# Kernel tuning notes

Hardware: AMD Instinct MI355X
Metric: run time of the kernel (lower is better)

Reference implementation:

```python
import jax, jax.numpy as jnp
import numpy as np

TOP_K = 8
NUM_EXPERTS = 256
NUM_GROUPS = 8
TOPK_GROUP = 4
SCALE = 2.5
EPS = 1e-20


def setup_inputs() -> dict:
    key = jax.random.key(0)
    k1, k2, k3 = jax.random.split(key, 3)
    T, H = 8192, 7168
    hidden_states = jax.random.normal(k1, (T, H), dtype=jnp.float32)
    # scale ~ kaiming-ish so logits are O(1) and sigmoid is not saturated
    weight = jax.random.normal(k2, (NUM_EXPERTS, H), dtype=jnp.float32) * (H ** -0.5)
    e_score_correction_bias = jax.random.normal(k3, (NUM_EXPERTS,), dtype=jnp.float32) * 0.1
    return {"hidden_states": hidden_states, "weight": weight,
            "e_score_correction_bias": e_score_correction_bias}


def reference(hidden_states, weight, e_score_correction_bias):
    T = hidden_states.shape[0]
    epg = NUM_EXPERTS // NUM_GROUPS  # experts per group
    # gating logits: [T, E]
    logits = jnp.einsum('th,eh->te', hidden_states.astype(jnp.float32),
                        weight.astype(jnp.float32))
    scores = jax.nn.sigmoid(logits)
    scores_for_choice = scores + e_score_correction_bias[None, :]
    # group score = sum of top-2 corrected scores within each group: [T, G]
    grouped = scores_for_choice.reshape(T, NUM_GROUPS, epg)
    top2, _ = jax.lax.top_k(grouped, 2)
    group_scores = top2.sum(axis=-1)
    # select topk_group groups, build mask [T, G]
    _, group_idx = jax.lax.top_k(group_scores, TOPK_GROUP)
    group_mask = jnp.zeros((T, NUM_GROUPS), dtype=scores.dtype)
    group_mask = group_mask.at[jnp.arange(T)[:, None], group_idx].set(1.0)
    # expand to expert mask [T, E]
    score_mask = jnp.repeat(group_mask, epg, axis=1)
    tmp_scores = jnp.where(score_mask > 0, scores_for_choice, 0.0)
    # top_k experts among allowed groups
    _, topk_idx = jax.lax.top_k(tmp_scores, TOP_K)
    # gather UNcorrected scores as weights
    topk_weight = jnp.take_along_axis(scores, topk_idx, axis=1)
    topk_weight = topk_weight / (topk_weight.sum(axis=-1, keepdims=True) + EPS)
    topk_weight = topk_weight * SCALE
    return topk_idx, topk_weight
```

## Files before the change

kernel.cpp:

```cpp
#include <hip/hip_runtime.h>
#include <cmath>

typedef __attribute__((ext_vector_type(8))) _Float16 half8;
typedef __attribute__((ext_vector_type(8))) unsigned short ushort8;
typedef __attribute__((ext_vector_type(4))) float f32x4;

#define HH 7168
#define NE 256
#define NQ 224
#define NITER 56
#define TOPK 8
#define TOPKG 4
#define WSC 1024.f
#define INV_WS (1.f/1024.f)
#define C1 (1.f/2048.f)
#define C2 (1.f/4194304.f)

__device__ __forceinline__ void split2(float x, unsigned short& h, unsigned short& m){
  const _Float16 hh = (_Float16)x;
  const float r = x - (float)hh;
  const _Float16 mm = (_Float16)(r * 2048.f);
  h = __builtin_bit_cast(unsigned short, hh);
  m = __builtin_bit_cast(unsigned short, mm);
}

__global__ __launch_bounds__(256) void prep_w(const float* __restrict__ wgt,
                                              unsigned short* __restrict__ bh,
                                              unsigned short* __restrict__ bm){
  const int b = blockIdx.x;
  const int nt = b & 15, qb = (b >> 4) * 4;
  const int w = threadIdx.x >> 6, L = threadIdx.x & 63;
  const int q = qb + w;
  const int e = nt*16 + (L & 15);
  const int k0 = 32*q + 8*(L >> 4);
  const float4 a0 = *(const float4*)(wgt + (size_t)e*HH + k0);
  const float4 a1 = *(const float4*)(wgt + (size_t)e*HH + k0 + 4);
  const float v[8] = {a0.x,a0.y,a0.z,a0.w,a1.x,a1.y,a1.z,a1.w};
  ushort8 h8, m8;
#pragma unroll
  for(int j=0;j<8;j++){ unsigned short hh,mm; split2(v[j]*WSC, hh, mm); h8[j]=hh; m8[j]=mm; }
  const size_t base = ((size_t)(q*16+nt)*64 + L)*8;
  *(ushort8*)(bh+base) = h8;
  *(ushort8*)(bm+base) = m8;
}

#define ABYTE(buf,lvl,mt,q,row) (((((buf)*2+(lvl))*8 + (mt)*4 + (q))*64 + (row))*16)
__device__ __forceinline__ int swz(int bo){ return bo ^ (((bo >> 8) & 7) << 4); }

__global__ __launch_bounds__(512,4)
void gemm(const float* __restrict__ hs,
          const unsigned short* __restrict__ bhp,
          const unsigned short* __restrict__ bmp,
          float* __restrict__ lgout){
  __shared__ __align__(16) unsigned short alds[16384];
  char* const aldsb = (char*)alds;

  const int tid = threadIdx.x, lane = tid & 63, w = tid >> 6;
  const int b = blockIdx.x;
  const int slice = (b >> 2) & 1;
  const int tg = (b >> 3)*4 + (b & 3);
  const int tb = tg*32, eb = slice*128;
  const int mtp = w >> 2, ntp = w & 3;

  const half8* __restrict__ bhv = (const half8*)bhp;
  const half8* __restrict__ bmv = (const half8*)bmp;

  f32x4 ksum[2], kcmp[2];
#pragma unroll
  for(int c=0;c<2;c++){ ksum[c]=f32x4{0,0,0,0}; kcmp[c]=f32x4{0,0,0,0}; }

  const int tokS = tid >> 4, kidx = tid & 15;
  const int mtS = tokS >> 4, m16S = tokS & 15;
  const int qS = kidx >> 2, kgS = kidx & 3;
  const int rowS = kgS*16 + m16S;
  const float* agp = hs + (size_t)(tb + tokS)*HH + kidx*8;

  float4 ga[2];
  ga[0] = *(const float4*)(agp);
  ga[1] = *(const float4*)(agp + 4);

  auto stage = [&](int buf){
    unsigned short h[8], m[8];
    const float* gv = (const float*)ga;
#pragma unroll
    for(int p=0;p<8;p++) split2(gv[p], h[p], m[p]);
    ushort8 h8, m8;
#pragma unroll
    for(int j=0;j<8;j++){ h8[j]=h[j]; m8[j]=m[j]; }
    *(ushort8*)(aldsb + swz(ABYTE(buf,0,mtS,qS,rowS))) = h8;
    *(ushort8*)(aldsb + swz(ABYTE(buf,1,mtS,qS,rowS))) = m8;
  };

  stage(0);
  half8 Bh[2], Bm[2];
#pragma unroll
  for(int ntl=0;ntl<2;ntl++){
    const int slot = ((0*16 + slice*8 + ntp*2 + ntl)*64 + lane);
    Bh[ntl] = bhv[slot]; Bm[ntl] = bmv[slot];
  }
  __syncthreads();

  for(int i=0;i<NITER;i++){
    const int cur = i & 1, nb = cur ^ 1;
    if(i+1 < NITER){
      const float* ap = agp + (size_t)(i+1)*128;
      ga[0] = *(const float4*)(ap);
      ga[1] = *(const float4*)(ap + 4);
    }
    f32x4 c0[2], c1[2], c2[2];
#pragma unroll
    for(int c=0;c<2;c++){ c0[c]=f32x4{0,0,0,0}; c1[c]=f32x4{0,0,0,0}; c2[c]=f32x4{0,0,0,0}; }

#pragma unroll
    for(int s=0;s<4;s++){
      const int q = i*4 + s;
      const half8 ah = *(const half8*)(aldsb + swz(ABYTE(cur,0,mtp,s,lane)));
      const half8 am = *(const half8*)(aldsb + swz(ABYTE(cur,1,mtp,s,lane)));
      half8 BhN[2], BmN[2];
      const bool more = (q+1 < NQ);
      if(more){
#pragma unroll
        for(int ntl=0;ntl<2;ntl++){
          const int slot = (((q+1)*16 + slice*8 + ntp*2 + ntl)*64 + lane);
          BhN[ntl] = bhv[slot]; BmN[ntl] = bmv[slot];
        }
      }
#pragma unroll
      for(int ntl=0;ntl<2;ntl++){
        c0[ntl] = __builtin_amdgcn_mfma_f32_16x16x32_f16(ah, Bh[ntl], c0[ntl], 0,0,0);
        c1[ntl] = __builtin_amdgcn_mfma_f32_16x16x32_f16(ah, Bm[ntl], c1[ntl], 0,0,0);
        c1[ntl] = __builtin_amdgcn_mfma_f32_16x16x32_f16(am, Bh[ntl], c1[ntl], 0,0,0);
        c2[ntl] = __builtin_amdgcn_mfma_f32_16x16x32_f16(am, Bm[ntl], c2[ntl], 0,0,0);
      }
      if(more){
#pragma unroll
        for(int ntl=0;ntl<2;ntl++){ Bh[ntl]=BhN[ntl]; Bm[ntl]=BmN[ntl]; }
      }
    }
    if(i+1 < NITER) stage(nb);
#pragma unroll
    for(int c=0;c<2;c++)
#pragma unroll
      for(int r=0;r<4;r++){
        const float v = c0[c][r] + c1[c][r]*C1 + c2[c][r]*C2;
        const float y = v - kcmp[c][r];
        const float t = ksum[c][r] + y;
        kcmp[c][r] = (t - ksum[c][r]) - y;
        ksum[c][r] = t;
      }
    __syncthreads();
  }

#pragma unroll
  for(int ntl=0;ntl<2;ntl++)
#pragma unroll
    for(int r=0;r<4;r++){
      const int tok = mtp*16 + (lane>>4)*4 + r;
      const int e = (ntp*2+ntl)*16 + (lane&15);
      const float lg = (ksum[ntl][r] - kcmp[ntl][r]) * INV_WS;
      lgout[(size_t)(tb+tok)*NE + eb + e] = lg;
    }
}

__global__ __launch_bounds__(256)
void gate(const float* __restrict__ lg, const float* __restrict__ bias,
          float* __restrict__ out, int T){
  const int tid = threadIdx.x, lane = tid & 63, wv = tid >> 6;
  const int t = blockIdx.x*4 + wv;
  const float4 bias4 = *(const float4*)(bias + 4*lane);
  const int g = lane >> 3;
  const float NEG_INF = -__builtin_inff();

  const float4 l4 = *(const float4*)(lg + (size_t)t*NE + 4*lane);
  float4 r4;
  r4.x = 1.f/(1.f + expf(-l4.x));
  r4.y = 1.f/(1.f + expf(-l4.y));
  r4.z = 1.f/(1.f + expf(-l4.z));
  r4.w = 1.f/(1.f + expf(-l4.w));
  float4 s4;
  s4.x = r4.x + bias4.x; s4.y = r4.y + bias4.y;
  s4.z = r4.z + bias4.z; s4.w = r4.w + bias4.w;

  float m1 = s4.x, m2 = NEG_INF;
  if (s4.y > m1) { m2 = m1; m1 = s4.y; } else if (s4.y > m2) m2 = s4.y;
  if (s4.z > m1) { m2 = m1; m1 = s4.z; } else if (s4.z > m2) m2 = s4.z;
  if (s4.w > m1) { m2 = m1; m1 = s4.w; } else if (s4.w > m2) m2 = s4.w;
#pragma unroll
  for (int m = 1; m <= 4; m <<= 1) {
    const float o1 = __shfl_xor(m1, m);
    const float o2 = __shfl_xor(m2, m);
    const float nm1 = fmaxf(m1, o1);
    const float nm2 = fmaxf(fminf(m1, o1), fmaxf(m2, o2));
    m1 = nm1; m2 = nm2;
  }
  const float gs = m1 + m2;

  float gsv[8];
#pragma unroll
  for (int j = 0; j < 8; ++j) gsv[j] = __shfl(gs, j * 8);

  unsigned gm = 0;
#pragma unroll
  for (int r = 0; r < TOPKG; ++r) {
    float best = NEG_INF; int bj = 0;
#pragma unroll
    for (int j = 0; j < 8; ++j) {
      const bool avail = !((gm >> j) & 1u);
      if (avail && gsv[j] > best) { best = gsv[j]; bj = j; }
    }
    gm |= 1u << bj;
  }
  const bool allowed = (gm >> g) & 1u;

  float v0 = allowed ? s4.x : 0.f;
  float v1 = allowed ? s4.y : 0.f;
  float v2 = allowed ? s4.z : 0.f;
  float v3 = allowed ? s4.w : 0.f;

  float sumw = 0.f;
  int myidx = 0; float myraw = 0.f;
#pragma unroll
  for (int r = 0; r < TOPK; ++r) {
    float bv = v0; int bj = 0;
    if (v1 > bv) { bv = v1; bj = 1; }
    if (v2 > bv) { bv = v2; bj = 2; }
    if (v3 > bv) { bv = v3; bj = 3; }
    int bidx = 4 * lane + bj;
#pragma unroll
    for (int m = 1; m < 64; m <<= 1) {
      const float ov = __shfl_xor(bv, m);
      const int   oi = __shfl_xor(bidx, m);
      if (ov > bv || (ov == bv && oi < bidx)) { bv = ov; bidx = oi; }
    }
    const int oj = bidx & 3;
    const float cand = (oj == 0) ? r4.x
                     : (oj == 1) ? r4.y
                     : (oj == 2) ? r4.z
                     :             r4.w;
    const float raw = __shfl(cand, bidx >> 2);
    sumw += raw;
    if (lane == r) { myidx = bidx; myraw = raw; }
    if (lane == (bidx >> 2)) {
      if      (oj == 0) v0 = NEG_INF;
      else if (oj == 1) v1 = NEG_INF;
      else if (oj == 2) v2 = NEG_INF;
      else              v3 = NEG_INF;
    }
  }

  if (lane < TOPK) {
    out[(size_t)t * TOPK + lane] = (float)myidx;
    out[(size_t)T * TOPK + (size_t)t * TOPK + lane] = myraw / (sumw + 1e-20f) * 2.5f;
  }
}

extern "C" void kernel_launch(void* const* d_in, const int* in_sizes, int n_in,
                              void* d_out, int out_size, void* d_ws, size_t ws_size,
                              hipStream_t stream) {
  const float* hs   = (const float*)d_in[0];
  const float* wgt  = (const float*)d_in[1];
  const float* bias = (const float*)d_in[2];
  float* out = (float*)d_out;

  const int T = in_sizes[0] / HH;

  unsigned short* bh = (unsigned short*)d_ws;
  unsigned short* bm = bh + (size_t)NE*HH;
  float* lgbuf = (float*)(bm + (size_t)NE*HH);

  hipLaunchKernelGGL(prep_w, dim3(896), dim3(256), 0, stream, wgt, bh, bm);
  hipLaunchKernelGGL(gemm,   dim3(512), dim3(512), 0, stream, hs, bh, bm, lgbuf);
  hipLaunchKernelGGL(gate,   dim3(T/4), dim3(256), 0, stream, lgbuf, bias, out, T);
}
```

Before: 465.2 us.

## Stage B operand through LDS via global_load_lds with finer K steps

The pre-split weight operand is now copied directly from global memory into a double-buffered 64KB LDS region with global_load_lds, and MFMA reads B from LDS instead of holding per-wave register prefetches. The K step per iteration is halved (NITER doubled), only half the threads convert and stage A, and MFMA sections are wrapped in s_setprio. The aim is to cut register pressure and redundant global B loads across waves, at the cost of much more LDS per block (80KB), which likely limits occupancy, and twice as many barriers.

After: 457.7 us. Within noise of the previous version (-1.6%).

```diff
diff --git a/kernel.cpp b/kernel.cpp
--- a/kernel.cpp
+++ b/kernel.cpp
@@ -8,7 +8,7 @@
 #define HH 7168
 #define NE 256
 #define NQ 224
-#define NITER 56
+#define NITER 112
 #define TOPK 8
 #define TOPKG 4
 #define WSC 1024.f
@@ -44,16 +44,23 @@
   *(ushort8*)(bm+base) = m8;
 }
 
-#define ABYTE(buf,lvl,mt,q,row) (((((buf)*2+(lvl))*8 + (mt)*4 + (q))*64 + (row))*16)
+#define ABYTE(buf,lvl,mt,q,row) ((((((buf)*2+(lvl))*2+(mt))*2+(q))*64+(row))*16)
+#define BBYTE(buf,lvl,q,nt) ((((buf)*4+(lvl)*2+(q))*8+(nt))<<10)
 __device__ __forceinline__ int swz(int bo){ return bo ^ (((bo >> 8) & 7) << 4); }
+
+__device__ __forceinline__ void glds16(const void* g, void* l){
+  __builtin_amdgcn_global_load_lds(
+      (const __attribute__((address_space(1))) unsigned int*)g,
+      (__attribute__((address_space(3))) unsigned int*)l, 16, 0, 0);
+}
 
 __global__ __launch_bounds__(512,4)
 void gemm(const float* __restrict__ hs,
           const unsigned short* __restrict__ bhp,
           const unsigned short* __restrict__ bmp,
           float* __restrict__ lgout){
-  __shared__ __align__(16) unsigned short alds[16384];
-  char* const aldsb = (char*)alds;
+  __shared__ __align__(16) unsigned char blds[65536];
+  __shared__ __align__(16) unsigned char alds[16384];
 
   const int tid = threadIdx.x, lane = tid & 63, w = tid >> 6;
   const int b = blockIdx.x;
@@ -62,69 +69,75 @@
   const int tb = tg*32, eb = slice*128;
   const int mtp = w >> 2, ntp = w & 3;
 
-  const half8* __restrict__ bhv = (const half8*)bhp;
-  const half8* __restrict__ bmv = (const half8*)bmp;
-
-  f32x4 ksum[2], kcmp[2];
+  f32x4 ksum[2], kcmp[2], c0[2], c1[2], c2[2];
 #pragma unroll
   for(int c=0;c<2;c++){ ksum[c]=f32x4{0,0,0,0}; kcmp[c]=f32x4{0,0,0,0}; }
 
-  const int tokS = tid >> 4, kidx = tid & 15;
+  const int tokS = (tid & 255) >> 3, kidx = tid & 7;
   const int mtS = tokS >> 4, m16S = tokS & 15;
   const int qS = kidx >> 2, kgS = kidx & 3;
   const int rowS = kgS*16 + m16S;
   const float* agp = hs + (size_t)(tb + tokS)*HH + kidx*8;
 
-  float4 ga[2];
-  ga[0] = *(const float4*)(agp);
-  ga[1] = *(const float4*)(agp + 4);
-
-  auto stage = [&](int buf){
+  auto stage = [&](int buf, const float4* g){
     unsigned short h[8], m[8];
-    const float* gv = (const float*)ga;
+    const float* gv = (const float*)g;
 #pragma unroll
     for(int p=0;p<8;p++) split2(gv[p], h[p], m[p]);
     ushort8 h8, m8;
 #pragma unroll
     for(int j=0;j<8;j++){ h8[j]=h[j]; m8[j]=m[j]; }
-    *(ushort8*)(aldsb + swz(ABYTE(buf,0,mtS,qS,rowS))) = h8;
-    *(ushort8*)(aldsb + swz(ABYTE(buf,1,mtS,qS,rowS))) = m8;
+    *(ushort8*)&alds[swz(ABYTE(buf,0,mtS,qS,rowS))] = h8;
+    *(ushort8*)&alds[swz(ABYTE(buf,1,mtS,qS,rowS))] = m8;
   };
 
-  stage(0);
-  half8 Bh[2], Bm[2];
-#pragma unroll
-  for(int ntl=0;ntl<2;ntl++){
-    const int slot = ((0*16 + slice*8 + ntp*2 + ntl)*64 + lane);
-    Bh[ntl] = bhv[slot]; Bm[ntl] = bmv[slot];
-  }
+  auto bstage = [&](int buf, int q32base){
+#pragma unroll
+    for(int j=0;j<4;j++){
+      const int sid = w*4 + j;
+      const int lvl = sid >> 4, q = (sid >> 3) & 1, nt = sid & 7;
+      const int q32 = q32base + q;
+      const unsigned short* src = (lvl ? bmp : bhp)
+          + ((size_t)((q32*16 + slice*8 + nt)*64 + lane))*8;
+      glds16(src, &blds[BBYTE(buf,lvl,q,nt)]);
+    }
+  };
+
+  float4 ga[2];
+  if(tid < 256){
+    ga[0] = *(const float4*)(agp);
+    ga[1] = *(const float4*)(agp + 4);
+  }
+  bstage(0, 0);
+  if(tid < 256) stage(0, ga);
   __syncthreads();
 
   for(int i=0;i<NITER;i++){
     const int cur = i & 1, nb = cur ^ 1;
-    if(i+1 < NITER){
-      const float* ap = agp + (size_t)(i+1)*128;
-      ga[0] = *(const float4*)(ap);
-      ga[1] = *(const float4*)(ap + 4);
-    }
-    f32x4 c0[2], c1[2], c2[2];
-#pragma unroll
-    for(int c=0;c<2;c++){ c0[c]=f32x4{0,0,0,0}; c1[c]=f32x4{0,0,0,0}; c2[c]=f32x4{0,0,0,0}; }
-
-#pragma unroll
-    for(int s=0;s<4;s++){
-      const int q = i*4 + s;
-      const half8 ah = *(const half8*)(aldsb + swz(ABYTE(cur,0,mtp,s,lane)));
-      const half8 am = *(const half8*)(aldsb + swz(ABYTE(cur,1,mtp,s,lane)));
-      half8 BhN[2], BmN[2];
-      const bool more = (q+1 < NQ);
-      if(more){
-#pragma unroll
-        for(int ntl=0;ntl<2;ntl++){
-          const int slot = (((q+1)*16 + slice*8 + ntp*2 + ntl)*64 + lane);
-          BhN[ntl] = bhv[slot]; BmN[ntl] = bmv[slot];
-        }
+    const bool more = (i+1 < NITER);
+    if(more){
+      if(tid < 256){
+        const float* ap = agp + (size_t)(i+1)*64;
+        ga[0] = *(const float4*)(ap);
+        ga[1] = *(const float4*)(ap + 4);
       }
+      bstage(nb, 2*(i+1));
+    }
+    if((i & 1) == 0){
+#pragma unroll
+      for(int c=0;c<2;c++){ c0[c]=f32x4{0,0,0,0}; c1[c]=f32x4{0,0,0,0}; c2[c]=f32x4{0,0,0,0}; }
+    }
+#pragma unroll
+    for(int s=0;s<2;s++){
+      const half8 ah = *(const half8*)&alds[swz(ABYTE(cur,0,mtp,s,lane))];
+      const half8 am = *(const half8*)&alds[swz(ABYTE(cur,1,mtp,s,lane))];
+      half8 Bh[2], Bm[2];
+#pragma unroll
+      for(int ntl=0;ntl<2;ntl++){
+        Bh[ntl] = *(const half8*)&blds[BBYTE(cur,0,s,ntp*2+ntl) + lane*16];
+        Bm[ntl] = *(const half8*)&blds[BBYTE(cur,1,s,ntp*2+ntl) + lane*16];
+      }
+      __builtin_amdgcn_s_setprio(1);
 #pragma unroll
       for(int ntl=0;ntl<2;ntl++){
         c0[ntl] = __builtin_amdgcn_mfma_f32_16x16x32_f16(ah, Bh[ntl], c0[ntl], 0,0,0);
@@ -132,22 +145,21 @@
         c1[ntl] = __builtin_amdgcn_mfma_f32_16x16x32_f16(am, Bh[ntl], c1[ntl], 0,0,0);
         c2[ntl] = __builtin_amdgcn_mfma_f32_16x16x32_f16(am, Bm[ntl], c2[ntl], 0,0,0);
       }
-      if(more){
-#pragma unroll
-        for(int ntl=0;ntl<2;ntl++){ Bh[ntl]=BhN[ntl]; Bm[ntl]=BmN[ntl]; }
-      }
-    }
-    if(i+1 < NITER) stage(nb);
-#pragma unroll
-    for(int c=0;c<2;c++)
-#pragma unroll
-      for(int r=0;r<4;r++){
-        const float v = c0[c][r] + c1[c][r]*C1 + c2[c][r]*C2;
-        const float y = v - kcmp[c][r];
-        const float t = ksum[c][r] + y;
-        kcmp[c][r] = (t - ksum[c][r]) - y;
-        ksum[c][r] = t;
-      }
+      __builtin_amdgcn_s_setprio(0);
+    }
+    if(more && tid < 256) stage(nb, ga);
+    if(i & 1){
+#pragma unroll
+      for(int c=0;c<2;c++)
+#pragma unroll
+        for(int r=0;r<4;r++){
+          const float v = c0[c][r] + c1[c][r]*C1 + c2[c][r]*C2;
+          const float y = v - kcmp[c][r];
+          const float t = ksum[c][r] + y;
+          kcmp[c][r] = (t - ksum[c][r]) - y;
+          ksum[c][r] = t;
+        }
+    }
     __syncthreads();
   }
 
```

## Stream B tiles into LDS via async global_load_lds with triple buffering

Applied to the files above, without the earlier changes.

The GEMM now loads the pre-split weight fragments (B) straight into shared memory with global_load_lds into a 3-stage ring buffer, instead of prefetching them into registers. Explicit vmcnt/lgkmcnt waits and raw barriers replace __syncthreads, and MFMA sections are wrapped in s_setprio. The aim is to hide global-load latency, cut register pressure and share B reads across waves through LDS. In exchange, LDS use grows to about 80KB per block, which may limit occupancy under launch_bounds(512,4), and the hand-written waitcnt sequencing could introduce races.

New measurement: 456.8 us. No clear change (-1.8%).

```diff
diff --git a/kernel.cpp b/kernel.cpp
--- a/kernel.cpp
+++ b/kernel.cpp
@@ -8,7 +8,7 @@
 #define HH 7168
 #define NE 256
 #define NQ 224
-#define NITER 56
+#define NWND 56
 #define TOPK 8
 #define TOPKG 4
 #define WSC 1024.f
@@ -44,16 +44,40 @@
   *(ushort8*)(bm+base) = m8;
 }
 
-#define ABYTE(buf,lvl,mt,q,row) (((((buf)*2+(lvl))*8 + (mt)*4 + (q))*64 + (row))*16)
+#define AB(aw,lvl,mt,q,row) (((((aw)*4+(lvl)*2+(mt))*4+(q))*64+(row))*16)
 __device__ __forceinline__ int swz(int bo){ return bo ^ (((bo >> 8) & 7) << 4); }
+
+__device__ __forceinline__ void glds16(const void* g, void* l){
+  __builtin_amdgcn_global_load_lds(
+      (const __attribute__((address_space(1))) unsigned int*)g,
+      (__attribute__((address_space(3))) unsigned int*)l, 16, 0, 0);
+}
+
+#define BAR_V4  do{ asm volatile("s_waitcnt vmcnt(4)" ::: "memory"); __builtin_amdgcn_s_barrier(); __builtin_amdgcn_sched_barrier(0); }while(0)
+#define BAR_V2  do{ asm volatile("s_waitcnt vmcnt(2)" ::: "memory"); __builtin_amdgcn_s_barrier(); __builtin_amdgcn_sched_barrier(0); }while(0)
+#define BAR_V2L do{ asm volatile("s_waitcnt lgkmcnt(0)\n\ts_waitcnt vmcnt(2)" ::: "memory"); __builtin_amdgcn_s_barrier(); __builtin_amdgcn_sched_barrier(0); }while(0)
+#define BAR_V0  do{ asm volatile("s_waitcnt vmcnt(0)" ::: "memory"); __builtin_amdgcn_s_barrier(); __builtin_amdgcn_sched_barrier(0); }while(0)
+
+#define KAHAN do{ \
+  _Pragma("unroll") \
+  for(int cc=0;cc<2;cc++) \
+    _Pragma("unroll") \
+    for(int r=0;r<4;r++){ \
+      const float v = c0[cc][r] + c1[cc][r]*C1 + c2[cc][r]*C2; \
+      const float y = v - kcmp[cc][r]; \
+      const float t = ksum[cc][r] + y; \
+      kcmp[cc][r] = (t - ksum[cc][r]) - y; \
+      ksum[cc][r] = t; \
+    } \
+}while(0)
 
 __global__ __launch_bounds__(512,4)
 void gemm(const float* __restrict__ hs,
           const unsigned short* __restrict__ bhp,
           const unsigned short* __restrict__ bmp,
           float* __restrict__ lgout){
-  __shared__ __align__(16) unsigned short alds[16384];
-  char* const aldsb = (char*)alds;
+  __shared__ __align__(16) unsigned char blds[49152];
+  __shared__ __align__(16) unsigned char alds[32768];
 
   const int tid = threadIdx.x, lane = tid & 63, w = tid >> 6;
   const int b = blockIdx.x;
@@ -62,24 +86,18 @@
   const int tb = tg*32, eb = slice*128;
   const int mtp = w >> 2, ntp = w & 3;
 
-  const half8* __restrict__ bhv = (const half8*)bhp;
-  const half8* __restrict__ bmv = (const half8*)bmp;
-
-  f32x4 ksum[2], kcmp[2];
-#pragma unroll
-  for(int c=0;c<2;c++){ ksum[c]=f32x4{0,0,0,0}; kcmp[c]=f32x4{0,0,0,0}; }
+  f32x4 ksum[2], kcmp[2], c0[2], c1[2], c2[2];
+#pragma unroll
+  for(int cc=0;cc<2;cc++){ ksum[cc]=f32x4{0,0,0,0}; kcmp[cc]=f32x4{0,0,0,0}; }
 
   const int tokS = tid >> 4, kidx = tid & 15;
   const int mtS = tokS >> 4, m16S = tokS & 15;
   const int qS = kidx >> 2, kgS = kidx & 3;
   const int rowS = kgS*16 + m16S;
   const float* agp = hs + (size_t)(tb + tokS)*HH + kidx*8;
-
   float4 ga[2];
-  ga[0] = *(const float4*)(agp);
-  ga[1] = *(const float4*)(agp + 4);
-
-  auto stage = [&](int buf){
+
+  auto stage = [&](int aw){
     unsigned short h[8], m[8];
     const float* gv = (const float*)ga;
 #pragma unroll
@@ -87,68 +105,99 @@
     ushort8 h8, m8;
 #pragma unroll
     for(int j=0;j<8;j++){ h8[j]=h[j]; m8[j]=m[j]; }
-    *(ushort8*)(aldsb + swz(ABYTE(buf,0,mtS,qS,rowS))) = h8;
-    *(ushort8*)(aldsb + swz(ABYTE(buf,1,mtS,qS,rowS))) = m8;
+    *(ushort8*)&alds[swz(AB(aw,0,mtS,qS,rowS))] = h8;
+    *(ushort8*)&alds[swz(AB(aw,1,mtS,qS,rowS))] = m8;
   };
 
+  const unsigned short* bsrc = (w >= 4 ? bmp : bhp)
+      + ((size_t)((slice*8 + (w&3)*2)*64 + lane))*8;
+  const int bdst = (w>>2)*8192 + (w&3)*2048;
+  auto issueB = [&](int bufoff, int qpre){
+    const unsigned short* s0 = bsrc + (size_t)qpre*8192;
+    glds16(s0,       &blds[bufoff + bdst]);
+    glds16(s0 + 512, &blds[bufoff + bdst + 1024]);
+  };
+
+  auto compute = [&](int awr, int q, int bc){
+    const half8 ah = *(const half8*)&alds[swz(AB(awr,0,mtp,q,lane))];
+    const half8 am = *(const half8*)&alds[swz(AB(awr,1,mtp,q,lane))];
+    half8 Bh[2], Bm[2];
+#pragma unroll
+    for(int ntl=0;ntl<2;ntl++){
+      Bh[ntl] = *(const half8*)&blds[bc + (ntp*2+ntl)*1024 + lane*16];
+      Bm[ntl] = *(const half8*)&blds[bc + 8192 + (ntp*2+ntl)*1024 + lane*16];
+    }
+    __builtin_amdgcn_s_setprio(1);
+#pragma unroll
+    for(int ntl=0;ntl<2;ntl++){
+      c0[ntl] = __builtin_amdgcn_mfma_f32_16x16x32_f16(ah, Bh[ntl], c0[ntl], 0,0,0);
+      c1[ntl] = __builtin_amdgcn_mfma_f32_16x16x32_f16(ah, Bm[ntl], c1[ntl], 0,0,0);
+      c1[ntl] = __builtin_amdgcn_mfma_f32_16x16x32_f16(am, Bh[ntl], c1[ntl], 0,0,0);
+      c2[ntl] = __builtin_amdgcn_mfma_f32_16x16x32_f16(am, Bm[ntl], c2[ntl], 0,0,0);
+    }
+    __builtin_amdgcn_s_setprio(0);
+  };
+
+  ga[0] = *(const float4*)agp; ga[1] = *(const float4*)(agp+4);
+  issueB(0,     0);
+  issueB(16384, 1);
   stage(0);
-  half8 Bh[2], Bm[2];
-#pragma unroll
-  for(int ntl=0;ntl<2;ntl++){
-    const int slot = ((0*16 + slice*8 + ntp*2 + ntl)*64 + lane);
-    Bh[ntl] = bhv[slot]; Bm[ntl] = bmv[slot];
-  }
-  __syncthreads();
-
-  for(int i=0;i<NITER;i++){
-    const int cur = i & 1, nb = cur ^ 1;
-    if(i+1 < NITER){
-      const float* ap = agp + (size_t)(i+1)*128;
-      ga[0] = *(const float4*)(ap);
-      ga[1] = *(const float4*)(ap + 4);
-    }
-    f32x4 c0[2], c1[2], c2[2];
-#pragma unroll
-    for(int c=0;c<2;c++){ c0[c]=f32x4{0,0,0,0}; c1[c]=f32x4{0,0,0,0}; c2[c]=f32x4{0,0,0,0}; }
-
-#pragma unroll
-    for(int s=0;s<4;s++){
-      const int q = i*4 + s;
-      const half8 ah = *(const half8*)(aldsb + swz(ABYTE(cur,0,mtp,s,lane)));
-      const half8 am = *(const half8*)(aldsb + swz(ABYTE(cur,1,mtp,s,lane)));
-      half8 BhN[2], BmN[2];
-      const bool more = (q+1 < NQ);
-      if(more){
-#pragma unroll
-        for(int ntl=0;ntl<2;ntl++){
-          const int slot = (((q+1)*16 + slice*8 + ntp*2 + ntl)*64 + lane);
-          BhN[ntl] = bhv[slot]; BmN[ntl] = bmv[slot];
-        }
-      }
-#pragma unroll
-      for(int ntl=0;ntl<2;ntl++){
-        c0[ntl] = __builtin_amdgcn_mfma_f32_16x16x32_f16(ah, Bh[ntl], c0[ntl], 0,0,0);
-        c1[ntl] = __builtin_amdgcn_mfma_f32_16x16x32_f16(ah, Bm[ntl], c1[ntl], 0,0,0);
-        c1[ntl] = __builtin_amdgcn_mfma_f32_16x16x32_f16(am, Bh[ntl], c1[ntl], 0,0,0);
-        c2[ntl] = __builtin_amdgcn_mfma_f32_16x16x32_f16(am, Bm[ntl], c2[ntl], 0,0,0);
-      }
-      if(more){
-#pragma unroll
-        for(int ntl=0;ntl<2;ntl++){ Bh[ntl]=BhN[ntl]; Bm[ntl]=BmN[ntl]; }
-      }
-    }
-    if(i+1 < NITER) stage(nb);
-#pragma unroll
-    for(int c=0;c<2;c++)
-#pragma unroll
-      for(int r=0;r<4;r++){
-        const float v = c0[c][r] + c1[c][r]*C1 + c2[c][r]*C2;
-        const float y = v - kcmp[c][r];
-        const float t = ksum[c][r] + y;
-        kcmp[c][r] = (t - ksum[c][r]) - y;
-        ksum[c][r] = t;
-      }
-    __syncthreads();
+  asm volatile("s_waitcnt lgkmcnt(0)\n\ts_waitcnt vmcnt(2)" ::: "memory");
+  __builtin_amdgcn_s_barrier();
+  __builtin_amdgcn_sched_barrier(0);
+
+  int bc = 0;
+#pragma unroll 1
+  for(int wnd=0; wnd<NWND-1; ++wnd){
+    const int i0 = wnd*4;
+    const int awr = wnd & 1, aws = awr ^ 1;
+    int bp;
+    bp = bc + 32768; if(bp >= 49152) bp -= 49152;
+    issueB(bp, i0+2);
+    { const float* ap = agp + (size_t)(wnd+1)*128;
+      ga[0] = *(const float4*)ap; ga[1] = *(const float4*)(ap+4); }
+#pragma unroll
+    for(int cc=0;cc<2;cc++){ c0[cc]=f32x4{0,0,0,0}; c1[cc]=f32x4{0,0,0,0}; c2[cc]=f32x4{0,0,0,0}; }
+    compute(awr, 0, bc);
+    BAR_V4;
+    bc += 16384; if(bc == 49152) bc = 0;
+    bp = bc + 32768; if(bp >= 49152) bp -= 49152;
+    issueB(bp, i0+3);
+    compute(awr, 1, bc);
+    BAR_V4;
+    bc += 16384; if(bc == 49152) bc = 0;
+    bp = bc + 32768; if(bp >= 49152) bp -= 49152;
+    issueB(bp, i0+4);
+    compute(awr, 2, bc);
+    stage(aws);
+    BAR_V2L;
+    bc += 16384; if(bc == 49152) bc = 0;
+    bp = bc + 32768; if(bp >= 49152) bp -= 49152;
+    issueB(bp, i0+5);
+    compute(awr, 3, bc);
+    KAHAN;
+    BAR_V2;
+    bc += 16384; if(bc == 49152) bc = 0;
+  }
+  {
+    int bp;
+    bp = bc + 32768; if(bp >= 49152) bp -= 49152;
+    issueB(bp, 222);
+#pragma unroll
+    for(int cc=0;cc<2;cc++){ c0[cc]=f32x4{0,0,0,0}; c1[cc]=f32x4{0,0,0,0}; c2[cc]=f32x4{0,0,0,0}; }
+    compute(1, 0, bc);
+    BAR_V2;
+    bc += 16384; if(bc == 49152) bc = 0;
+    bp = bc + 32768; if(bp >= 49152) bp -= 49152;
+    issueB(bp, 223);
+    compute(1, 1, bc);
+    BAR_V2;
+    bc += 16384; if(bc == 49152) bc = 0;
+    compute(1, 2, bc);
+    BAR_V0;
+    bc += 16384; if(bc == 49152) bc = 0;
+    compute(1, 3, bc);
+    KAHAN;
   }
 
 #pragma unroll
```

## Halve K-step per barrier, ping-pong B prefetch, and prioritize MFMA issue

Applied to the files above, without the earlier changes.

Each main-loop iteration now covers 64 K elements instead of 128, so the LDS A buffer holds two K-subtiles per stage instead of four. The loop count doubles and the Kahan accumulation runs every other iteration. B fragments are double-buffered in named registers (PA/PB) so the next subtile's global loads are issued before the current MFMAs run. MFMA groups are wrapped in s_setprio, and the full __syncthreads is replaced by an explicit lgkmcnt wait plus s_barrier, with the loop kept rolled. The aim is lower register and LDS pressure and better load/compute overlap, at the cost of twice as many barriers per K.

After: 486.2 us. +4.5%, slower.

```diff
diff --git a/kernel.cpp b/kernel.cpp
--- a/kernel.cpp
+++ b/kernel.cpp
@@ -8,7 +8,7 @@
 #define HH 7168
 #define NE 256
 #define NQ 224
-#define NITER 56
+#define NITER 112
 #define TOPK 8
 #define TOPKG 4
 #define WSC 1024.f
@@ -44,16 +44,41 @@
   *(ushort8*)(bm+base) = m8;
 }
 
-#define ABYTE(buf,lvl,mt,q,row) (((((buf)*2+(lvl))*8 + (mt)*4 + (q))*64 + (row))*16)
+#define AB(buf,lvl,mt,q,row) ((((((buf)*2+(lvl))*2+(mt))*2+(q))*64+(row))*16)
 __device__ __forceinline__ int swz(int bo){ return bo ^ (((bo >> 8) & 7) << 4); }
+
+#define KAHAN do{ \
+  _Pragma("unroll") \
+  for(int cc=0;cc<2;cc++) \
+    _Pragma("unroll") \
+    for(int r=0;r<4;r++){ \
+      const float v = c0[cc][r] + c1[cc][r]*C1 + c2[cc][r]*C2; \
+      const float y = v - kcmp[cc][r]; \
+      const float t = ksum[cc][r] + y; \
+      kcmp[cc][r] = (t - ksum[cc][r]) - y; \
+      ksum[cc][r] = t; \
+    } \
+}while(0)
+
+#define MFMA8(AH,AM,BH0,BH1,BM0,BM1) do{ \
+  __builtin_amdgcn_s_setprio(1); \
+  c0[0] = __builtin_amdgcn_mfma_f32_16x16x32_f16(AH, BH0, c0[0], 0,0,0); \
+  c1[0] = __builtin_amdgcn_mfma_f32_16x16x32_f16(AH, BM0, c1[0], 0,0,0); \
+  c1[0] = __builtin_amdgcn_mfma_f32_16x16x32_f16(AM, BH0, c1[0], 0,0,0); \
+  c2[0] = __builtin_amdgcn_mfma_f32_16x16x32_f16(AM, BM0, c2[0], 0,0,0); \
+  c0[1] = __builtin_amdgcn_mfma_f32_16x16x32_f16(AH, BH1, c0[1], 0,0,0); \
+  c1[1] = __builtin_amdgcn_mfma_f32_16x16x32_f16(AH, BM1, c1[1], 0,0,0); \
+  c1[1] = __builtin_amdgcn_mfma_f32_16x16x32_f16(AM, BH1, c1[1], 0,0,0); \
+  c2[1] = __builtin_amdgcn_mfma_f32_16x16x32_f16(AM, BM1, c2[1], 0,0,0); \
+  __builtin_amdgcn_s_setprio(0); \
+}while(0)
 
 __global__ __launch_bounds__(512,4)
 void gemm(const float* __restrict__ hs,
           const unsigned short* __restrict__ bhp,
           const unsigned short* __restrict__ bmp,
           float* __restrict__ lgout){
-  __shared__ __align__(16) unsigned short alds[16384];
-  char* const aldsb = (char*)alds;
+  __shared__ __align__(16) unsigned char alds[16384];
 
   const int tid = threadIdx.x, lane = tid & 63, w = tid >> 6;
   const int b = blockIdx.x;
@@ -62,22 +87,16 @@
   const int tb = tg*32, eb = slice*128;
   const int mtp = w >> 2, ntp = w & 3;
 
-  const half8* __restrict__ bhv = (const half8*)bhp;
-  const half8* __restrict__ bmv = (const half8*)bmp;
-
-  f32x4 ksum[2], kcmp[2];
-#pragma unroll
-  for(int c=0;c<2;c++){ ksum[c]=f32x4{0,0,0,0}; kcmp[c]=f32x4{0,0,0,0}; }
-
-  const int tokS = tid >> 4, kidx = tid & 15;
+  f32x4 ksum[2], kcmp[2], c0[2], c1[2], c2[2];
+#pragma unroll
+  for(int cc=0;cc<2;cc++){ ksum[cc]=f32x4{0,0,0,0}; kcmp[cc]=f32x4{0,0,0,0}; }
+
+  const int tokS = (tid & 255) >> 3, kidx = tid & 7;
   const int mtS = tokS >> 4, m16S = tokS & 15;
   const int qS = kidx >> 2, kgS = kidx & 3;
   const int rowS = kgS*16 + m16S;
   const float* agp = hs + (size_t)(tb + tokS)*HH + kidx*8;
-
   float4 ga[2];
-  ga[0] = *(const float4*)(agp);
-  ga[1] = *(const float4*)(agp + 4);
 
   auto stage = [&](int buf){
     unsigned short h[8], m[8];
@@ -87,68 +106,62 @@
     ushort8 h8, m8;
 #pragma unroll
     for(int j=0;j<8;j++){ h8[j]=h[j]; m8[j]=m[j]; }
-    *(ushort8*)(aldsb + swz(ABYTE(buf,0,mtS,qS,rowS))) = h8;
-    *(ushort8*)(aldsb + swz(ABYTE(buf,1,mtS,qS,rowS))) = m8;
+    *(ushort8*)&alds[swz(AB(buf,0,mtS,qS,rowS))] = h8;
+    *(ushort8*)&alds[swz(AB(buf,1,mtS,qS,rowS))] = m8;
   };
 
+  const half8* __restrict__ bhv = (const half8*)bhp;
+  const half8* __restrict__ bmv = (const half8*)bmp;
+  const int bbase0 = (slice*8 + ntp*2)*64 + lane;
+  const int bbase1 = bbase0 + 64;
+
+  ga[0] = *(const float4*)(agp);
+  ga[1] = *(const float4*)(agp + 4);
   stage(0);
-  half8 Bh[2], Bm[2];
-#pragma unroll
-  for(int ntl=0;ntl<2;ntl++){
-    const int slot = ((0*16 + slice*8 + ntp*2 + ntl)*64 + lane);
-    Bh[ntl] = bhv[slot]; Bm[ntl] = bmv[slot];
-  }
-  __syncthreads();
-
+  half8 PAh0 = bhv[bbase0], PAh1 = bhv[bbase1];
+  half8 PAm0 = bmv[bbase0], PAm1 = bmv[bbase1];
+  asm volatile("s_waitcnt lgkmcnt(0)" ::: "memory");
+  __builtin_amdgcn_s_barrier();
+
+  half8 PBh0, PBh1, PBm0, PBm1;
+
+#pragma unroll 1
   for(int i=0;i<NITER;i++){
     const int cur = i & 1, nb = cur ^ 1;
-    if(i+1 < NITER){
-      const float* ap = agp + (size_t)(i+1)*128;
+    const bool more = (i+1 < NITER);
+    if(more){
+      const float* ap = agp + (size_t)(i+1)*64;
       ga[0] = *(const float4*)(ap);
       ga[1] = *(const float4*)(ap + 4);
     }
-    f32x4 c0[2], c1[2], c2[2];
-#pragma unroll
-    for(int c=0;c<2;c++){ c0[c]=f32x4{0,0,0,0}; c1[c]=f32x4{0,0,0,0}; c2[c]=f32x4{0,0,0,0}; }
-
-#pragma unroll
-    for(int s=0;s<4;s++){
-      const int q = i*4 + s;
-      const half8 ah = *(const half8*)(aldsb + swz(ABYTE(cur,0,mtp,s,lane)));
-      const half8 am = *(const half8*)(aldsb + swz(ABYTE(cur,1,mtp,s,lane)));
-      half8 BhN[2], BmN[2];
-      const bool more = (q+1 < NQ);
-      if(more){
-#pragma unroll
-        for(int ntl=0;ntl<2;ntl++){
-          const int slot = (((q+1)*16 + slice*8 + ntp*2 + ntl)*64 + lane);
-          BhN[ntl] = bhv[slot]; BmN[ntl] = bmv[slot];
-        }
-      }
-#pragma unroll
-      for(int ntl=0;ntl<2;ntl++){
-        c0[ntl] = __builtin_amdgcn_mfma_f32_16x16x32_f16(ah, Bh[ntl], c0[ntl], 0,0,0);
-        c1[ntl] = __builtin_amdgcn_mfma_f32_16x16x32_f16(ah, Bm[ntl], c1[ntl], 0,0,0);
-        c1[ntl] = __builtin_amdgcn_mfma_f32_16x16x32_f16(am, Bh[ntl], c1[ntl], 0,0,0);
-        c2[ntl] = __builtin_amdgcn_mfma_f32_16x16x32_f16(am, Bm[ntl], c2[ntl], 0,0,0);
-      }
-      if(more){
-#pragma unroll
-        for(int ntl=0;ntl<2;ntl++){ Bh[ntl]=BhN[ntl]; Bm[ntl]=BmN[ntl]; }
-      }
-    }
-    if(i+1 < NITER) stage(nb);
-#pragma unroll
-    for(int c=0;c<2;c++)
-#pragma unroll
-      for(int r=0;r<4;r++){
-        const float v = c0[c][r] + c1[c][r]*C1 + c2[c][r]*C2;
-        const float y = v - kcmp[c][r];
-        const float t = ksum[c][r] + y;
-        kcmp[c][r] = (t - ksum[c][r]) - y;
-        ksum[c][r] = t;
-      }
-    __syncthreads();
+    if((i & 1) == 0){
+#pragma unroll
+      for(int cc=0;cc<2;cc++){ c0[cc]=f32x4{0,0,0,0}; c1[cc]=f32x4{0,0,0,0}; c2[cc]=f32x4{0,0,0,0}; }
+    }
+    {
+      const int s1 = (2*i+1)*1024;
+      PBh0 = bhv[s1 + bbase0]; PBh1 = bhv[s1 + bbase1];
+      PBm0 = bmv[s1 + bbase0]; PBm1 = bmv[s1 + bbase1];
+    }
+    {
+      const half8 ah = *(const half8*)&alds[swz(AB(cur,0,mtp,0,lane))];
+      const half8 am = *(const half8*)&alds[swz(AB(cur,1,mtp,0,lane))];
+      MFMA8(ah, am, PAh0, PAh1, PAm0, PAm1);
+    }
+    if(more){
+      const int s2 = (2*i+2)*1024;
+      PAh0 = bhv[s2 + bbase0]; PAh1 = bhv[s2 + bbase1];
+      PAm0 = bmv[s2 + bbase0]; PAm1 = bmv[s2 + bbase1];
+    }
+    {
+      const half8 ah = *(const half8*)&alds[swz(AB(cur,0,mtp,1,lane))];
+      const half8 am = *(const half8*)&alds[swz(AB(cur,1,mtp,1,lane))];
+      MFMA8(ah, am, PBh0, PBh1, PBm0, PBm1);
+    }
+    if(more) stage(nb);
+    if(i & 1) KAHAN;
+    asm volatile("s_waitcnt lgkmcnt(0)" ::: "memory");
+    __builtin_amdgcn_s_barrier();
   }
 
 #pragma unroll
```
